# Optimization experiments

Measured on AMD Instinct MI355X. Metric: run time of the kernel, lower is better.

## Reference

```python
import jax, jax.numpy as jnp
import numpy as np

EPS = 1e-5  # BatchNorm eps

def _gcn_norm(edge_index, edge_weight, n):
    # PyG gcn_norm with add_self_loops=True, fill_value=1.0
    loop = jnp.arange(n, dtype=edge_index.dtype)
    row = jnp.concatenate([edge_index[0], loop])
    col = jnp.concatenate([edge_index[1], loop])
    ew = jnp.concatenate([edge_weight, jnp.ones((n,), edge_weight.dtype)])
    deg = jax.ops.segment_sum(ew, col, num_segments=n)
    dis = jnp.where(deg > 0, jax.lax.rsqrt(jnp.maximum(deg, 1e-30)), 0.0)
    norm = dis[row] * ew * dis[col]
    return row, col, norm

def _gcn_conv(x, W, b, row, col, norm, n):
    h = x @ W                               # [N, out]
    msg = h[row] * norm[:, None]            # gather + edge scale
    out = jax.ops.segment_sum(msg, col, num_segments=n)
    return out + b

def _bn_eval(x, gamma, beta, mean, var):
    return (x - mean) * jax.lax.rsqrt(var + EPS) * gamma + beta

def setup_inputs() -> dict:
    key = jax.random.key(0)
    ks = jax.random.split(key, 12)
    N, E, V, H = 100000, 1600000, 256, 128
    x = jax.random.normal(ks[0], (N, V), jnp.float32)
    edge_index = jax.random.randint(ks[1], (2, E), 0, N, jnp.int64)
    edge_weight = jax.random.uniform(ks[2], (E,), jnp.float32)
    s = lambda fan: 1.0 / np.sqrt(fan)
    return {
        "x": x, "edge_index": edge_index, "edge_weight": edge_weight,
        "W1": jax.random.normal(ks[3], (V, H), jnp.float32) * s(V),
        "b1": jnp.zeros((H,), jnp.float32),
        "W2": jax.random.normal(ks[4], (H, H), jnp.float32) * s(H),
        "b2": jnp.zeros((H,), jnp.float32),
        "W3": jax.random.normal(ks[5], (H, 1), jnp.float32) * s(H),
        "b3": jnp.zeros((1,), jnp.float32),
        "Wres": jax.random.normal(ks[6], (V, H), jnp.float32) * s(V),
        "g1": jnp.ones((H,), jnp.float32), "be1": jnp.zeros((H,), jnp.float32),
        "m1": jax.random.normal(ks[7], (H,), jnp.float32) * 0.01,
        "v1": jnp.ones((H,), jnp.float32),
        "g2": jnp.ones((H,), jnp.float32), "be2": jnp.zeros((H,), jnp.float32),
        "m2": jax.random.normal(ks[8], (H,), jnp.float32) * 0.01,
        "v2": jnp.ones((H,), jnp.float32),
    }

def reference(x, edge_index, edge_weight, W1, b1, W2, b2, W3, b3, Wres,
              g1, be1, m1, v1, g2, be2, m2, v2):
    n = x.shape[0]
    row, col, norm = _gcn_norm(edge_index, edge_weight, n)
    res = x @ Wres                                   # residual branch
    h = _gcn_conv(x, W1, b1, row, col, norm, n)
    h = jax.nn.relu(_bn_eval(h, g1, be1, m1, v1))    # dropout off (eval)
    h = _gcn_conv(h, W2, b2, row, col, norm, n) + res
    h = jax.nn.relu(_bn_eval(h, g2, be2, m2, v2))
    h = _gcn_conv(h, W3, b3, row, col, norm, n)      # [N, 1]
    return jnp.squeeze(h, axis=1)
```

## Files before the change

kernel.cpp:

```cpp
#include <hip/hip_runtime.h>
#include <hip/hip_bf16.h>

#define BN_EPS 1e-5f

using short8 = __attribute__((ext_vector_type(8))) short;
using f32x4  = __attribute__((ext_vector_type(4))) float;

#define FIX_SCALE 262144.0f
#define FIX_MASK  0x01ffffffu
#define CNT_ONE   (1u << 25)

static __device__ __forceinline__ unsigned short f2bf(float f) {
  unsigned int u = __float_as_uint(f);
  unsigned int r = (u + 0x7fffu + ((u >> 16) & 1u)) >> 16;
  return (unsigned short)r;
}


static __global__ void cast_weights(const float* __restrict__ W1, const float* __restrict__ Wres,
                                    const float* __restrict__ W2,
                                    unsigned short* __restrict__ B2,
                                    unsigned short* __restrict__ BT2) {
  int i = blockIdx.x * blockDim.x + threadIdx.x;
  if (i < 256 * 256) {
    int n = i >> 8, k = i & 255;
    float v = (n < 128) ? W1[k * 128 + n] : Wres[k * 128 + (n - 128)];
    B2[(k >> 5) * 8192 + n * 32 + (k & 31)] = f2bf(v);
  } else if (i < 256 * 256 + 128 * 128) {
    int j = i - 256 * 256;
    int n = j >> 7, k = j & 127;
    BT2[j] = f2bf(W2[k * 128 + n]);
  }
}


static __global__ __launch_bounds__(256)
void fused_gemm1_hist(const float* __restrict__ A, const unsigned short* __restrict__ B2,
                      unsigned short* __restrict__ C0, unsigned short* __restrict__ C1, int M,
                      const int* __restrict__ col, const float* __restrict__ ew,
                      unsigned int* __restrict__ packed,
                      unsigned short* __restrict__ rank, int E, int hB, int N) {
  __shared__ unsigned short As[2 * 64 * 40];

  int b = blockIdx.x;
  if (b < hB) {
    unsigned int xcc;
    asm volatile("s_getreg_b32 %0, hwreg(HW_REG_XCC_ID)" : "=s"(xcc));
    xcc &= 7u;
    unsigned int* mytab = packed + (size_t)xcc * N;
    int base = b * (256 * 8) + threadIdx.x;
#pragma unroll
    for (int j = 0; j < 8; ++j) {
      int e = base + j * 256;
      if (e < E) {
        int c = col[e];
        unsigned int fx = (unsigned int)(ew[e] * FIX_SCALE + 0.5f);
        unsigned int old = __hip_atomic_fetch_add(&mytab[c], CNT_ONE | fx,
                                                  __ATOMIC_RELAXED,
                                                  __HIP_MEMORY_SCOPE_WORKGROUP);
        rank[e] = (unsigned short)(((old >> 25) & 0x1fffu) | (xcc << 13));
      }
    }
    return;
  }

  int t = threadIdx.x;
  int wv = t >> 6, lane = t & 63;
  int quad = lane >> 4, l15 = lane & 15;
  int m0 = (b - hB) * 64;

  f32x4 acc[4][4];
#pragma unroll
  for (int i = 0; i < 4; ++i)
#pragma unroll
    for (int j = 0; j < 4; ++j) acc[i][j] = (f32x4){0.f, 0.f, 0.f, 0.f};

  int ar = t >> 2;
  int ac = (t & 3) * 8;
  bool avalid = (m0 + ar) < M;
  const float* Arow = A + (size_t)(m0 + ar) * 256 + ac;
  const unsigned short* Bfrag = B2 + (wv * 64 + l15) * 32 + quad * 8;

  float4 a0 = make_float4(0.f, 0.f, 0.f, 0.f), a1 = a0;
  if (avalid) {
    a0 = *(const float4*)(Arow + 0);
    a1 = *(const float4*)(Arow + 4);
  }
  {
    short8 av;
    av[0] = (short)f2bf(a0.x); av[1] = (short)f2bf(a0.y);
    av[2] = (short)f2bf(a0.z); av[3] = (short)f2bf(a0.w);
    av[4] = (short)f2bf(a1.x); av[5] = (short)f2bf(a1.y);
    av[6] = (short)f2bf(a1.z); av[7] = (short)f2bf(a1.w);
    *(short8*)&As[ar * 40 + ac] = av;
  }
  short8 bc[4];
#pragma unroll
  for (int nt = 0; nt < 4; ++nt)
    bc[nt] = *(const short8*)(Bfrag + nt * 512);
  __syncthreads();

#pragma unroll 2
  for (int s = 0; s < 8; ++s) {
    int cur = (s & 1) ? 2560 : 0;

    short8 bn[4];
    if (s < 7) {
#pragma unroll
      for (int nt = 0; nt < 4; ++nt)
        bn[nt] = *(const short8*)(Bfrag + (s + 1) * 8192 + nt * 512);
      if (avalid) {
        a0 = *(const float4*)(Arow + (s + 1) * 32);
        a1 = *(const float4*)(Arow + (s + 1) * 32 + 4);
      }
    }

    short8 af[4];
#pragma unroll
    for (int mt = 0; mt < 4; ++mt)
      af[mt] = *(const short8*)&As[cur + (mt * 16 + l15) * 40 + quad * 8];
#pragma unroll
    for (int mt = 0; mt < 4; ++mt)
#pragma unroll
      for (int nt = 0; nt < 4; ++nt)
        acc[mt][nt] = __builtin_amdgcn_mfma_f32_16x16x32_bf16(af[mt], bc[nt], acc[mt][nt], 0, 0, 0);

    if (s < 7) {
      short8 av;
      av[0] = (short)f2bf(a0.x); av[1] = (short)f2bf(a0.y);
      av[2] = (short)f2bf(a0.z); av[3] = (short)f2bf(a0.w);
      av[4] = (short)f2bf(a1.x); av[5] = (short)f2bf(a1.y);
      av[6] = (short)f2bf(a1.z); av[7] = (short)f2bf(a1.w);
      *(short8*)&As[(cur ^ 2560) + ar * 40 + ac] = av;
#pragma unroll
      for (int nt = 0; nt < 4; ++nt) bc[nt] = bn[nt];
    }
    __syncthreads();
  }

  int nbase = wv * 64;
#pragma unroll
  for (int mt = 0; mt < 4; ++mt) {
#pragma unroll
    for (int nt = 0; nt < 4; ++nt) {
      int n = nbase + nt * 16 + l15;
#pragma unroll
      for (int reg = 0; reg < 4; ++reg) {
        size_t m = (size_t)(m0 + mt * 16 + quad * 4 + reg);
        if (nbase < 128) C0[m * 128 + n] = f2bf(acc[mt][nt][reg]);
        else             C1[m * 128 + (n - 128)] = f2bf(acc[mt][nt][reg]);
      }
    }
  }
}


#define SCAN_B 256
#define SCAN_I 16
static __global__ void scanA(const unsigned int* __restrict__ packed,
                             float* __restrict__ dis, int* __restrict__ cnt,
                             int* __restrict__ startV, int* __restrict__ blkSum, int N) {
  __shared__ int sh[SCAN_B];
  int t = threadIdx.x;
  int vbase = blockIdx.x * (SCAN_B * SCAN_I) + t * SCAN_I;
  int v[SCAN_I];
  int tot = 0;
#pragma unroll
  for (int g = 0; g < 2; ++g) {
    int c = (vbase >> 3) + g;
    int csum = 0;
    if (c < N) {
      unsigned int usum = 0;
#pragma unroll
      for (int r = 0; r < 8; ++r) {
        unsigned int pv = packed[(size_t)r * N + c];
        int cr = (int)(pv >> 25);
        v[g * 8 + r] = cr;
        csum += cr;
        usum += (pv & FIX_MASK);
      }
      cnt[c] = csum;
      dis[c] = rsqrtf(1.0f + (float)usum * (1.0f / FIX_SCALE));
    } else {
#pragma unroll
      for (int r = 0; r < 8; ++r) v[g * 8 + r] = 0;
    }
    tot += csum;
  }
  sh[t] = tot;
  __syncthreads();
  int self = tot;
  for (int off = 1; off < SCAN_B; off <<= 1) {
    int add = (t >= off) ? sh[t - off] : 0;
    __syncthreads();
    sh[t] += add;
    __syncthreads();
  }
  int excl = sh[t] - self;
  if (t == SCAN_B - 1) blkSum[blockIdx.x] = sh[t];
  int run = excl;
#pragma unroll
  for (int j = 0; j < SCAN_I; ++j) {
    if (vbase + j < 8 * N) startV[vbase + j] = run;
    run += v[j];
  }
}

static __global__ void scanB(const int* __restrict__ blkSum, int* __restrict__ blkOff, int nb) {
  __shared__ int sh[256];
  int t = threadIdx.x;
  int v = (t < nb) ? blkSum[t] : 0;
  sh[t] = v;
  __syncthreads();
  for (int off = 1; off < 256; off <<= 1) {
    int add = (t >= off) ? sh[t - off] : 0;
    __syncthreads();
    sh[t] += add;
    __syncthreads();
  }
  if (t < nb) blkOff[t] = sh[t] - v;
}

static __global__ void place_kernel(const int* __restrict__ row, const int* __restrict__ col,
                                    const float* __restrict__ ew, const float* __restrict__ dis,
                                    const int* __restrict__ startV, const int* __restrict__ blkOff,
                                    const unsigned short* __restrict__ rank,
                                    long long* __restrict__ edges, int E) {
  int e = blockIdx.x * blockDim.x + threadIdx.x;
  if (e < E) {
    int r = row[e], c = col[e];
    unsigned int rk = rank[e];
    int vv = c * 8 + (int)(rk >> 13);
    int pos = startV[vv] + blkOff[vv >> 12] + (int)(rk & 0x1fffu);
    float nrm = dis[r] * ew[e];
    long long v = ((long long)__float_as_int(nrm) << 32) | (unsigned int)r;
    __builtin_nontemporal_store(v, &edges[pos]);
  }
}


static __global__ __launch_bounds__(256)
void gemm2_mfma(const unsigned short* __restrict__ A, const unsigned short* __restrict__ BT,
                unsigned short* __restrict__ C) {
  __shared__ unsigned short As[128 * 40];
  __shared__ unsigned short Bs[128 * 40];
  int t = threadIdx.x;
  int wv = t >> 6, lane = t & 63;
  int quad = lane >> 4, l15 = lane & 15;
  int m0 = blockIdx.x * 128;

  f32x4 acc[4][4];
#pragma unroll
  for (int i = 0; i < 4; ++i)
#pragma unroll
    for (int j = 0; j < 4; ++j) acc[i][j] = (f32x4){0.f, 0.f, 0.f, 0.f};

  int sr = t >> 1, sc = (t & 1) * 16;

  for (int k0 = 0; k0 < 128; k0 += 32) {
    short8 a0 = *(const short8*)(A + (size_t)(m0 + sr) * 128 + k0 + sc);
    short8 a1 = *(const short8*)(A + (size_t)(m0 + sr) * 128 + k0 + sc + 8);
    *(short8*)&As[sr * 40 + sc]     = a0;
    *(short8*)&As[sr * 40 + sc + 8] = a1;
    short8 b0 = *(const short8*)(BT + (size_t)sr * 128 + k0 + sc);
    short8 b1 = *(const short8*)(BT + (size_t)sr * 128 + k0 + sc + 8);
    *(short8*)&Bs[sr * 40 + sc]     = b0;
    *(short8*)&Bs[sr * 40 + sc + 8] = b1;
    __syncthreads();

    int mb = (wv >> 1) * 64, nb = (wv & 1) * 64;
    short8 af[4], bf[4];
#pragma unroll
    for (int mt = 0; mt < 4; ++mt)
      af[mt] = *(const short8*)&As[(mb + mt * 16 + l15) * 40 + quad * 8];
#pragma unroll
    for (int nt = 0; nt < 4; ++nt)
      bf[nt] = *(const short8*)&Bs[(nb + nt * 16 + l15) * 40 + quad * 8];
#pragma unroll
    for (int mt = 0; mt < 4; ++mt)
#pragma unroll
      for (int nt = 0; nt < 4; ++nt)
        acc[mt][nt] = __builtin_amdgcn_mfma_f32_16x16x32_bf16(af[mt], bf[nt], acc[mt][nt], 0, 0, 0);
    __syncthreads();
  }

  int mb = (wv >> 1) * 64, nb = (wv & 1) * 64;
#pragma unroll
  for (int mt = 0; mt < 4; ++mt)
#pragma unroll
    for (int nt = 0; nt < 4; ++nt) {
      int n = nb + nt * 16 + l15;
#pragma unroll
      for (int reg = 0; reg < 4; ++reg) {
        size_t m = (size_t)(m0 + mb + mt * 16 + quad * 4 + reg);
        C[m * 128 + n] = f2bf(acc[mt][nt][reg]);
      }
    }
}


#define PROP_GATHER_BODY                                                        \
  int c0 = lane * 2;                                                            \
  float d = dis[w];                                                             \
  float acc0, acc1;                                                             \
  {                                                                             \
    unsigned int u = Hsrc[(size_t)w * 64 + lane];                               \
    acc0 = d * __uint_as_float(u << 16);                                        \
    acc1 = d * __uint_as_float(u & 0xffff0000u);                                \
  }                                                                             \
  int s = start8[(size_t)w * 8] + blkOff[w >> 9], n = cnt[w];                   \
  int k = 0;                                                                    \
  while (k < n) {                                                               \
    int chunk = min(n - k, 64);                                                 \
    int idx = 0;                                                                \
    float wt = 0.f;                                                             \
    if (lane < chunk) {                                                         \
      long long ev = edges[s + k + lane];                                       \
      idx = (int)(unsigned int)(ev & 0xffffffffLL);                             \
      wt  = __int_as_float((int)(ev >> 32));                                    \
    }                                                                           \
    for (int j = 0; j < chunk; j += 8) {                                        \
      int   i0 = __shfl(idx, j + 0, 64), i1 = __shfl(idx, j + 1, 64);           \
      int   i2 = __shfl(idx, j + 2, 64), i3 = __shfl(idx, j + 3, 64);           \
      int   i4 = __shfl(idx, j + 4, 64), i5 = __shfl(idx, j + 5, 64);           \
      int   i6 = __shfl(idx, j + 6, 64), i7 = __shfl(idx, j + 7, 64);           \
      float w0 = __shfl(wt, j + 0, 64), w1 = __shfl(wt, j + 1, 64);             \
      float w2 = __shfl(wt, j + 2, 64), w3 = __shfl(wt, j + 3, 64);             \
      float w4 = __shfl(wt, j + 4, 64), w5 = __shfl(wt, j + 5, 64);             \
      float w6 = __shfl(wt, j + 6, 64), w7 = __shfl(wt, j + 7, 64);             \
      unsigned int u0 = Hsrc[(size_t)i0 * 64 + lane];                           \
      unsigned int u1 = Hsrc[(size_t)i1 * 64 + lane];                           \
      unsigned int u2 = Hsrc[(size_t)i2 * 64 + lane];                           \
      unsigned int u3 = Hsrc[(size_t)i3 * 64 + lane];                           \
      unsigned int u4 = Hsrc[(size_t)i4 * 64 + lane];                           \
      unsigned int u5 = Hsrc[(size_t)i5 * 64 + lane];                           \
      unsigned int u6 = Hsrc[(size_t)i6 * 64 + lane];                           \
      unsigned int u7 = Hsrc[(size_t)i7 * 64 + lane];                           \
      acc0 = fmaf(w0, __uint_as_float(u0 << 16), acc0);                         \
      acc1 = fmaf(w0, __uint_as_float(u0 & 0xffff0000u), acc1);                 \
      acc0 = fmaf(w1, __uint_as_float(u1 << 16), acc0);                         \
      acc1 = fmaf(w1, __uint_as_float(u1 & 0xffff0000u), acc1);                 \
      acc0 = fmaf(w2, __uint_as_float(u2 << 16), acc0);                         \
      acc1 = fmaf(w2, __uint_as_float(u2 & 0xffff0000u), acc1);                 \
      acc0 = fmaf(w3, __uint_as_float(u3 << 16), acc0);                         \
      acc1 = fmaf(w3, __uint_as_float(u3 & 0xffff0000u), acc1);                 \
      acc0 = fmaf(w4, __uint_as_float(u4 << 16), acc0);                         \
      acc1 = fmaf(w4, __uint_as_float(u4 & 0xffff0000u), acc1);                 \
      acc0 = fmaf(w5, __uint_as_float(u5 << 16), acc0);                         \
      acc1 = fmaf(w5, __uint_as_float(u5 & 0xffff0000u), acc1);                 \
      acc0 = fmaf(w6, __uint_as_float(u6 << 16), acc0);                         \
      acc1 = fmaf(w6, __uint_as_float(u6 & 0xffff0000u), acc1);                 \
      acc0 = fmaf(w7, __uint_as_float(u7 << 16), acc0);                         \
      acc1 = fmaf(w7, __uint_as_float(u7 & 0xffff0000u), acc1);                 \
    }                                                                           \
    k += chunk;                                                                 \
  }                                                                             \
  acc0 *= d;                                                                    \
  acc1 *= d;

static __global__ __launch_bounds__(256)
void prop128_bf16out(const unsigned int* __restrict__ Hsrc,
                     const int* __restrict__ start8, const int* __restrict__ blkOff,
                     const int* __restrict__ cnt,
                     const long long* __restrict__ edges,
                     const float* __restrict__ dis,
                     const float* __restrict__ bvec,
                     const float* __restrict__ g, const float* __restrict__ be,
                     const float* __restrict__ mean, const float* __restrict__ var,
                     unsigned int* __restrict__ Outb, int N) {
  int w = (int)((blockIdx.x * blockDim.x + threadIdx.x) >> 6);
  int lane = threadIdx.x & 63;
  if (w >= N) return;
  PROP_GATHER_BODY
  float x0 = acc0 + bvec[c0];
  float x1 = acc1 + bvec[c0 + 1];
  float s0 = g[c0] * rsqrtf(var[c0] + BN_EPS);
  float s1 = g[c0 + 1] * rsqrtf(var[c0 + 1] + BN_EPS);
  x0 = fmaxf((x0 - mean[c0]) * s0 + be[c0], 0.f);
  x1 = fmaxf((x1 - mean[c0 + 1]) * s1 + be[c0 + 1], 0.f);
  unsigned int packed = (unsigned int)f2bf(x0) | ((unsigned int)f2bf(x1) << 16);
  Outb[(size_t)w * 64 + lane] = packed;
}

static __global__ __launch_bounds__(256)
void prop128_w3out(const unsigned int* __restrict__ Hsrc,
                   const int* __restrict__ start8, const int* __restrict__ blkOff,
                   const int* __restrict__ cnt,
                   const long long* __restrict__ edges,
                   const float* __restrict__ dis,
                   const float* __restrict__ bvec,
                   const float* __restrict__ g, const float* __restrict__ be,
                   const float* __restrict__ mean, const float* __restrict__ var,
                   const unsigned int* __restrict__ resb, const float* __restrict__ W3,
                   float* __restrict__ h3, int N) {
  int w = (int)((blockIdx.x * blockDim.x + threadIdx.x) >> 6);
  int lane = threadIdx.x & 63;
  if (w >= N) return;
  PROP_GATHER_BODY
  unsigned int ru = resb[(size_t)w * 64 + lane];
  float x0 = acc0 + bvec[c0]     + __uint_as_float(ru << 16);
  float x1 = acc1 + bvec[c0 + 1] + __uint_as_float(ru & 0xffff0000u);
  float s0 = g[c0] * rsqrtf(var[c0] + BN_EPS);
  float s1 = g[c0 + 1] * rsqrtf(var[c0 + 1] + BN_EPS);
  x0 = fmaxf((x0 - mean[c0]) * s0 + be[c0], 0.f);
  x1 = fmaxf((x1 - mean[c0 + 1]) * s1 + be[c0 + 1], 0.f);
  float v = x0 * W3[c0] + x1 * W3[c0 + 1];
#pragma unroll
  for (int off = 32; off > 0; off >>= 1) v += __shfl_down(v, off, 64);
  if (lane == 0) h3[w] = v;
}


static __global__ __launch_bounds__(256)
void prop3_kernel(const float* __restrict__ h3,
                  const int* __restrict__ start8, const int* __restrict__ blkOff,
                  const int* __restrict__ cnt,
                  const long long* __restrict__ edges,
                  const float* __restrict__ dis, const float* __restrict__ b3,
                  float* __restrict__ out, int N) {
  int tid = blockIdx.x * blockDim.x + threadIdx.x;
  int i = tid >> 2;
  int sub = tid & 3;
  if (i >= N) return;
  float acc = 0.f;
  int s = start8[(size_t)i * 8] + blkOff[i >> 9], n = cnt[i];
  for (int k = sub; k < n; k += 4) {
    long long ev = edges[s + k];
    int src = (int)(unsigned int)(ev & 0xffffffffLL);
    float wt = __int_as_float((int)(ev >> 32));
    acc = fmaf(wt, h3[src], acc);
  }
  acc += __shfl_xor(acc, 1, 64);
  acc += __shfl_xor(acc, 2, 64);
  if (sub == 0) {
    float d = dis[i];
    out[i] = (acc + d * h3[i]) * d + b3[0];
  }
}


extern "C" void kernel_launch(void* const* d_in, const int* in_sizes, int n_in,
                              void* d_out, int out_size, void* d_ws, size_t ws_size,
                              hipStream_t stream) {
  const float* x    = (const float*)d_in[0];
  const int*   ei   = (const int*)d_in[1];
  const float* ew   = (const float*)d_in[2];
  const float* W1   = (const float*)d_in[3];
  const float* b1   = (const float*)d_in[4];
  const float* W2   = (const float*)d_in[5];
  const float* b2   = (const float*)d_in[6];
  const float* W3   = (const float*)d_in[7];
  const float* b3   = (const float*)d_in[8];
  const float* Wres = (const float*)d_in[9];
  const float* g1   = (const float*)d_in[10];
  const float* be1  = (const float*)d_in[11];
  const float* m1   = (const float*)d_in[12];
  const float* v1   = (const float*)d_in[13];
  const float* g2   = (const float*)d_in[14];
  const float* be2  = (const float*)d_in[15];
  const float* m2   = (const float*)d_in[16];
  const float* v2   = (const float*)d_in[17];

  int Hh = in_sizes[4];
  int V  = in_sizes[3] / Hh;
  int N  = in_sizes[0] / V;
  int E  = in_sizes[2];
  const int* row = ei;
  const int* col = ei + E;

  int Mp = ((N + 127) / 128) * 128;

  char* p = (char*)d_ws;
  auto alloc = [&](size_t bytes) -> char* {
    char* r = p;
    p += (bytes + 255) & ~(size_t)255;
    return r;
  };
  unsigned int* packed = (unsigned int*)alloc((size_t)N * 8 * 4);
  float* dis    = (float*)alloc((size_t)N * 4);
  int*   cnt    = (int*)  alloc((size_t)N * 4);
  int*   startV = (int*)  alloc((size_t)N * 8 * 4);
  int*   blkSum = (int*)  alloc(256 * 4);
  int*   blkOff = (int*)  alloc(256 * 4);
  unsigned short* rank = (unsigned short*)alloc((size_t)E * 2);
  long long* edges = (long long*)alloc((size_t)E * 8);
  float* h3     = (float*)alloc((size_t)N * 4);
  unsigned short* B2  = (unsigned short*)alloc((size_t)256 * 256 * 2);
  unsigned short* BT2 = (unsigned short*)alloc((size_t)128 * 128 * 2);
  unsigned short* bufG  = (unsigned short*)alloc((size_t)Mp * 128 * 2);
  unsigned short* bufH1 = (unsigned short*)alloc((size_t)Mp * 128 * 2);
  unsigned short* bufRes = (unsigned short*)alloc((size_t)Mp * 128 * 2);
  (void)ws_size; (void)n_in; (void)out_size;

  int TB = 256;
  hipMemsetAsync(packed, 0, (size_t)N * 8 * 4, stream);
  cast_weights<<<(256 * 256 + 128 * 128 + TB - 1) / TB, TB, 0, stream>>>(W1, Wres, W2, B2, BT2);

  int hB = (E + TB * 8 - 1) / (TB * 8);
  int gB = Mp / 64;
  fused_gemm1_hist<<<hB + gB, TB, 0, stream>>>(x, B2, bufG, bufRes, N,
                                               col, ew, packed, rank, E, hB, N);

  int NV = 8 * N;
  int nb = (NV + SCAN_B * SCAN_I - 1) / (SCAN_B * SCAN_I);
  scanA<<<nb, SCAN_B, 0, stream>>>(packed, dis, cnt, startV, blkSum, N);
  scanB<<<1, 256, 0, stream>>>(blkSum, blkOff, nb);
  place_kernel<<<(E + TB - 1) / TB, TB, 0, stream>>>(row, col, ew, dis, startV, blkOff,
                                                     rank, edges, E);

  int propBlocks = (int)(((size_t)N * 64 + TB - 1) / TB);
  prop128_bf16out<<<propBlocks, TB, 0, stream>>>((const unsigned int*)bufG, startV, blkOff, cnt,
                                                 edges, dis, b1, g1, be1, m1, v1,
                                                 (unsigned int*)bufH1, N);

  gemm2_mfma<<<Mp / 128, 256, 0, stream>>>(bufH1, BT2, bufG);

  prop128_w3out<<<propBlocks, TB, 0, stream>>>((const unsigned int*)bufG, startV, blkOff, cnt,
                                               edges, dis, b2, g2, be2, m2, v2,
                                               (const unsigned int*)bufRes, W3, h3, N);

  prop3_kernel<<<(int)(((size_t)N * 4 + TB - 1) / TB), TB, 0, stream>>>(h3, startV, blkOff, cnt,
                                                                        edges, dis, b3,
                                                                        (float*)d_out, N);
}
```

Before: 483.3 us.

## Replace global-atomic CSR build with two-level bucket sort via LDS counting

The per-XCC global atomic histogram with rank tracking is replaced by a two-level counting sort. Per-block LDS histograms over 128-node buckets are reduced and prefix-scanned, then edges are scattered into buckets. Each bucket is sorted locally into CSR order in LDS, computing degree and dis along the way, and a final pass writes the normalized weights. This removes contended global atomics and the large packed/startV arrays, at the cost of more kernel launches and an extra E-sized temporary pass. It also relies on row indices fitting in 17 bits.

Result: faster. 454.2 us (-6.0%).

```diff
diff --git a/kernel.cpp b/kernel.cpp
--- a/kernel.cpp
+++ b/kernel.cpp
@@ -2,13 +2,13 @@
 #include <hip/hip_bf16.h>
 
 #define BN_EPS 1e-5f
+#define FIX_SCALE 262144.0f
+
+#define EPB 2048
+#define NBK_MAX 816
 
 using short8 = __attribute__((ext_vector_type(8))) short;
 using f32x4  = __attribute__((ext_vector_type(4))) float;
-
-#define FIX_SCALE 262144.0f
-#define FIX_MASK  0x01ffffffu
-#define CNT_ONE   (1u << 25)
 
 static __device__ __forceinline__ unsigned short f2bf(float f) {
   unsigned int u = __float_as_uint(f);
@@ -35,39 +35,32 @@
 
 
 static __global__ __launch_bounds__(256)
-void fused_gemm1_hist(const float* __restrict__ A, const unsigned short* __restrict__ B2,
-                      unsigned short* __restrict__ C0, unsigned short* __restrict__ C1, int M,
-                      const int* __restrict__ col, const float* __restrict__ ew,
-                      unsigned int* __restrict__ packed,
-                      unsigned short* __restrict__ rank, int E, int hB, int N) {
+void fused_count_gemm1(const float* __restrict__ A, const unsigned short* __restrict__ B2,
+                       unsigned short* __restrict__ C0, unsigned short* __restrict__ C1, int M,
+                       const int* __restrict__ col, int* __restrict__ BB,
+                       int E, int CB, int NBK) {
   __shared__ unsigned short As[2 * 64 * 40];
 
   int b = blockIdx.x;
-  if (b < hB) {
-    unsigned int xcc;
-    asm volatile("s_getreg_b32 %0, hwreg(HW_REG_XCC_ID)" : "=s"(xcc));
-    xcc &= 7u;
-    unsigned int* mytab = packed + (size_t)xcc * N;
-    int base = b * (256 * 8) + threadIdx.x;
+  int t = threadIdx.x;
+  if (b < CB) {
+    unsigned int* cnts = (unsigned int*)As;
+    for (int k = t; k < NBK; k += 256) cnts[k] = 0u;
+    __syncthreads();
+    int base = b * EPB + t;
 #pragma unroll
     for (int j = 0; j < 8; ++j) {
       int e = base + j * 256;
-      if (e < E) {
-        int c = col[e];
-        unsigned int fx = (unsigned int)(ew[e] * FIX_SCALE + 0.5f);
-        unsigned int old = __hip_atomic_fetch_add(&mytab[c], CNT_ONE | fx,
-                                                  __ATOMIC_RELAXED,
-                                                  __HIP_MEMORY_SCOPE_WORKGROUP);
-        rank[e] = (unsigned short)(((old >> 25) & 0x1fffu) | (xcc << 13));
-      }
-    }
+      if (e < E) atomicAdd(&cnts[col[e] >> 7], 1u);
+    }
+    __syncthreads();
+    for (int k = t; k < NBK; k += 256) BB[(size_t)b * NBK + k] = (int)cnts[k];
     return;
   }
 
-  int t = threadIdx.x;
   int wv = t >> 6, lane = t & 63;
   int quad = lane >> 4, l15 = lane & 15;
-  int m0 = (b - hB) * 64;
+  int m0 = (b - CB) * 64;
 
   f32x4 acc[4][4];
 #pragma unroll
@@ -155,86 +148,162 @@
 }
 
 
-#define SCAN_B 256
-#define SCAN_I 16
-static __global__ void scanA(const unsigned int* __restrict__ packed,
-                             float* __restrict__ dis, int* __restrict__ cnt,
-                             int* __restrict__ startV, int* __restrict__ blkSum, int N) {
-  __shared__ int sh[SCAN_B];
-  int t = threadIdx.x;
-  int vbase = blockIdx.x * (SCAN_B * SCAN_I) + t * SCAN_I;
-  int v[SCAN_I];
-  int tot = 0;
-#pragma unroll
-  for (int g = 0; g < 2; ++g) {
-    int c = (vbase >> 3) + g;
-    int csum = 0;
+static __global__ void totals_kernel(const int* __restrict__ BB, int* __restrict__ total,
+                                     int CB, int NBK) {
+  __shared__ int sh[256];
+  int k = blockIdx.x;
+  int t = threadIdx.x;
+  int part = 0;
+  for (int b = t; b < CB; b += 256) part += BB[(size_t)b * NBK + k];
+  sh[t] = part;
+  __syncthreads();
+  for (int off = 128; off > 0; off >>= 1) {
+    if (t < off) sh[t] += sh[t + off];
+    __syncthreads();
+  }
+  if (t == 0) total[k] = sh[0];
+}
+
+static __global__ void base_kernel(const int* __restrict__ total, int* __restrict__ bucketBase,
+                                   int NBK) {
+  __shared__ int sh[256];
+  __shared__ int carrySh;
+  int t = threadIdx.x;
+  if (t == 0) carrySh = 0;
+  __syncthreads();
+  for (int c0 = 0; c0 < NBK; c0 += 256) {
+    int i = c0 + t;
+    int v = (i < NBK) ? total[i] : 0;
+    sh[t] = v;
+    __syncthreads();
+    for (int off = 1; off < 256; off <<= 1) {
+      int add = (t >= off) ? sh[t - off] : 0;
+      __syncthreads();
+      sh[t] += add;
+      __syncthreads();
+    }
+    if (i < NBK) bucketBase[i] = carrySh + sh[t] - v;
+    __syncthreads();
+    if (t == 0) carrySh += sh[255];
+    __syncthreads();
+  }
+  if (t == 0) bucketBase[NBK] = carrySh;
+}
+
+static __global__ void off_kernel(int* __restrict__ BB, const int* __restrict__ bucketBase,
+                                  int CB, int NBK) {
+  __shared__ int sh[256];
+  __shared__ int carrySh;
+  int k = blockIdx.x;
+  int t = threadIdx.x;
+  if (t == 0) carrySh = bucketBase[k];
+  __syncthreads();
+  for (int b0 = 0; b0 < CB; b0 += 256) {
+    int b = b0 + t;
+    int v = (b < CB) ? BB[(size_t)b * NBK + k] : 0;
+    sh[t] = v;
+    __syncthreads();
+    for (int off = 1; off < 256; off <<= 1) {
+      int add = (t >= off) ? sh[t - off] : 0;
+      __syncthreads();
+      sh[t] += add;
+      __syncthreads();
+    }
+    if (b < CB) BB[(size_t)b * NBK + k] = carrySh + sh[t] - v;
+    __syncthreads();
+    if (t == 0) carrySh += sh[255];
+    __syncthreads();
+  }
+}
+
+static __global__ void scatter_kernel(const int* __restrict__ row, const int* __restrict__ col,
+                                      const float* __restrict__ ew, const int* __restrict__ BB,
+                                      unsigned long long* __restrict__ tmp, int E, int NBK) {
+  __shared__ unsigned int cur[NBK_MAX];
+  int b = blockIdx.x;
+  int t = threadIdx.x;
+  for (int k = t; k < NBK; k += 256) cur[k] = (unsigned int)BB[(size_t)b * NBK + k];
+  __syncthreads();
+  int base = b * EPB + t;
+#pragma unroll
+  for (int j = 0; j < 8; ++j) {
+    int e = base + j * 256;
+    if (e < E) {
+      int c = col[e];
+      int k = c >> 7;
+      unsigned int pos = atomicAdd(&cur[k], 1u);
+      unsigned int lo = (unsigned int)row[e] | ((unsigned int)(c & 127) << 17);
+      unsigned long long w = ((unsigned long long)__float_as_uint(ew[e]) << 32) | lo;
+      tmp[pos] = w;
+    }
+  }
+}
+
+static __global__ void bucket_csr(const unsigned long long* __restrict__ tmp,
+                                  const int* __restrict__ bucketBase,
+                                  int* __restrict__ cnt, int* __restrict__ start,
+                                  float* __restrict__ dis,
+                                  unsigned long long* __restrict__ edges, int N) {
+  __shared__ unsigned int colCnt[128];
+  __shared__ unsigned int sumEw[128];
+  __shared__ int so[128];
+  int k = blockIdx.x;
+  int t = threadIdx.x;
+  int segBase = bucketBase[k], segEnd = bucketBase[k + 1];
+  int segN = segEnd - segBase;
+
+  if (t < 128) { colCnt[t] = 0u; sumEw[t] = 0u; }
+  __syncthreads();
+
+  for (int i = t; i < segN; i += 256) {
+    unsigned long long w = tmp[segBase + i];
+    unsigned int lo = (unsigned int)w;
+    int cl = (int)((lo >> 17) & 127u);
+    float ewv = __uint_as_float((unsigned int)(w >> 32));
+    atomicAdd(&colCnt[cl], 1u);
+    atomicAdd(&sumEw[cl], (unsigned int)(ewv * FIX_SCALE + 0.5f));
+  }
+  __syncthreads();
+
+  if (t < 128) so[t] = (int)colCnt[t];
+  __syncthreads();
+  for (int off = 1; off < 128; off <<= 1) {
+    int add = (t >= off && t < 128) ? so[t - off] : 0;
+    __syncthreads();
+    if (t < 128) so[t] += add;
+    __syncthreads();
+  }
+
+  if (t < 128) {
+    int excl = so[t] - (int)colCnt[t];
+    int c = k * 128 + t;
     if (c < N) {
-      unsigned int usum = 0;
-#pragma unroll
-      for (int r = 0; r < 8; ++r) {
-        unsigned int pv = packed[(size_t)r * N + c];
-        int cr = (int)(pv >> 25);
-        v[g * 8 + r] = cr;
-        csum += cr;
-        usum += (pv & FIX_MASK);
-      }
-      cnt[c] = csum;
-      dis[c] = rsqrtf(1.0f + (float)usum * (1.0f / FIX_SCALE));
-    } else {
-#pragma unroll
-      for (int r = 0; r < 8; ++r) v[g * 8 + r] = 0;
-    }
-    tot += csum;
-  }
-  sh[t] = tot;
-  __syncthreads();
-  int self = tot;
-  for (int off = 1; off < SCAN_B; off <<= 1) {
-    int add = (t >= off) ? sh[t - off] : 0;
-    __syncthreads();
-    sh[t] += add;
-    __syncthreads();
-  }
-  int excl = sh[t] - self;
-  if (t == SCAN_B - 1) blkSum[blockIdx.x] = sh[t];
-  int run = excl;
-#pragma unroll
-  for (int j = 0; j < SCAN_I; ++j) {
-    if (vbase + j < 8 * N) startV[vbase + j] = run;
-    run += v[j];
-  }
-}
-
-static __global__ void scanB(const int* __restrict__ blkSum, int* __restrict__ blkOff, int nb) {
-  __shared__ int sh[256];
-  int t = threadIdx.x;
-  int v = (t < nb) ? blkSum[t] : 0;
-  sh[t] = v;
-  __syncthreads();
-  for (int off = 1; off < 256; off <<= 1) {
-    int add = (t >= off) ? sh[t - off] : 0;
-    __syncthreads();
-    sh[t] += add;
-    __syncthreads();
-  }
-  if (t < nb) blkOff[t] = sh[t] - v;
-}
-
-static __global__ void place_kernel(const int* __restrict__ row, const int* __restrict__ col,
-                                    const float* __restrict__ ew, const float* __restrict__ dis,
-                                    const int* __restrict__ startV, const int* __restrict__ blkOff,
-                                    const unsigned short* __restrict__ rank,
-                                    long long* __restrict__ edges, int E) {
-  int e = blockIdx.x * blockDim.x + threadIdx.x;
-  if (e < E) {
-    int r = row[e], c = col[e];
-    unsigned int rk = rank[e];
-    int vv = c * 8 + (int)(rk >> 13);
-    int pos = startV[vv] + blkOff[vv >> 12] + (int)(rk & 0x1fffu);
-    float nrm = dis[r] * ew[e];
-    long long v = ((long long)__float_as_int(nrm) << 32) | (unsigned int)r;
-    __builtin_nontemporal_store(v, &edges[pos]);
+      cnt[c] = (int)colCnt[t];
+      start[c] = segBase + excl;
+      dis[c] = rsqrtf(1.0f + (float)sumEw[t] * (1.0f / FIX_SCALE));
+    }
+    colCnt[t] = (unsigned int)excl;
+  }
+  __syncthreads();
+
+  for (int i = t; i < segN; i += 256) {
+    unsigned long long w = tmp[segBase + i];
+    unsigned int lo = (unsigned int)w;
+    int cl = (int)((lo >> 17) & 127u);
+    unsigned int p = atomicAdd(&colCnt[cl], 1u);
+    edges[segBase + (int)p] = (w & 0xffffffff00000000ull) | (unsigned long long)(lo & 0x1ffffu);
+  }
+}
+
+static __global__ void finalize_kernel(unsigned long long* __restrict__ edges,
+                                       const float* __restrict__ dis, int E) {
+  int i = blockIdx.x * blockDim.x + threadIdx.x;
+  if (i < E) {
+    unsigned long long w = edges[i];
+    int r = (int)(unsigned int)(w & 0xffffffffull);
+    float ewv = __uint_as_float((unsigned int)(w >> 32));
+    float nrm = dis[r] * ewv;
+    edges[i] = ((unsigned long long)__float_as_uint(nrm) << 32) | (unsigned int)r;
   }
 }
 
@@ -308,14 +377,14 @@
     acc0 = d * __uint_as_float(u << 16);                                        \
     acc1 = d * __uint_as_float(u & 0xffff0000u);                                \
   }                                                                             \
-  int s = start8[(size_t)w * 8] + blkOff[w >> 9], n = cnt[w];                   \
+  int s = start[w], n = cnt[w];                                                 \
   int k = 0;                                                                    \
   while (k < n) {                                                               \
     int chunk = min(n - k, 64);                                                 \
     int idx = 0;                                                                \
     float wt = 0.f;                                                             \
     if (lane < chunk) {                                                         \
-      long long ev = edges[s + k + lane];                                       \
+      long long ev = (long long)edges[s + k + lane];                            \
       idx = (int)(unsigned int)(ev & 0xffffffffLL);                             \
       wt  = __int_as_float((int)(ev >> 32));                                    \
     }                                                                           \
@@ -360,9 +429,8 @@
 
 static __global__ __launch_bounds__(256)
 void prop128_bf16out(const unsigned int* __restrict__ Hsrc,
-                     const int* __restrict__ start8, const int* __restrict__ blkOff,
-                     const int* __restrict__ cnt,
-                     const long long* __restrict__ edges,
+                     const int* __restrict__ start, const int* __restrict__ cnt,
+                     const unsigned long long* __restrict__ edges,
                      const float* __restrict__ dis,
                      const float* __restrict__ bvec,
                      const float* __restrict__ g, const float* __restrict__ be,
@@ -384,9 +452,8 @@
 
 static __global__ __launch_bounds__(256)
 void prop128_w3out(const unsigned int* __restrict__ Hsrc,
-                   const int* __restrict__ start8, const int* __restrict__ blkOff,
-                   const int* __restrict__ cnt,
-                   const long long* __restrict__ edges,
+                   const int* __restrict__ start, const int* __restrict__ cnt,
+                   const unsigned long long* __restrict__ edges,
                    const float* __restrict__ dis,
                    const float* __restrict__ bvec,
                    const float* __restrict__ g, const float* __restrict__ be,
@@ -413,9 +480,8 @@
 
 static __global__ __launch_bounds__(256)
 void prop3_kernel(const float* __restrict__ h3,
-                  const int* __restrict__ start8, const int* __restrict__ blkOff,
-                  const int* __restrict__ cnt,
-                  const long long* __restrict__ edges,
+                  const int* __restrict__ start, const int* __restrict__ cnt,
+                  const unsigned long long* __restrict__ edges,
                   const float* __restrict__ dis, const float* __restrict__ b3,
                   float* __restrict__ out, int N) {
   int tid = blockIdx.x * blockDim.x + threadIdx.x;
@@ -423,11 +489,11 @@
   int sub = tid & 3;
   if (i >= N) return;
   float acc = 0.f;
-  int s = start8[(size_t)i * 8] + blkOff[i >> 9], n = cnt[i];
+  int s = start[i], n = cnt[i];
   for (int k = sub; k < n; k += 4) {
-    long long ev = edges[s + k];
-    int src = (int)(unsigned int)(ev & 0xffffffffLL);
-    float wt = __int_as_float((int)(ev >> 32));
+    unsigned long long ev = edges[s + k];
+    int src = (int)(unsigned int)(ev & 0xffffffffull);
+    float wt = __uint_as_float((unsigned int)(ev >> 32));
     acc = fmaf(wt, h3[src], acc);
   }
   acc += __shfl_xor(acc, 1, 64);
@@ -469,6 +535,8 @@
   const int* col = ei + E;
 
   int Mp = ((N + 127) / 128) * 128;
+  int CB  = (E + EPB - 1) / EPB;
+  int NBK = (N + 127) >> 7;
 
   char* p = (char*)d_ws;
   auto alloc = [&](size_t bytes) -> char* {
@@ -476,14 +544,14 @@
     p += (bytes + 255) & ~(size_t)255;
     return r;
   };
-  unsigned int* packed = (unsigned int*)alloc((size_t)N * 8 * 4);
+  int*   BB     = (int*)alloc((size_t)CB * NBK * 4);
+  int*   total  = (int*)alloc((size_t)NBK * 4);
+  int*   bucketBase = (int*)alloc((size_t)(NBK + 1) * 4);
   float* dis    = (float*)alloc((size_t)N * 4);
   int*   cnt    = (int*)  alloc((size_t)N * 4);
-  int*   startV = (int*)  alloc((size_t)N * 8 * 4);
-  int*   blkSum = (int*)  alloc(256 * 4);
-  int*   blkOff = (int*)  alloc(256 * 4);
-  unsigned short* rank = (unsigned short*)alloc((size_t)E * 2);
-  long long* edges = (long long*)alloc((size_t)E * 8);
+  int*   startA = (int*)  alloc((size_t)N * 4);
+  unsigned long long* tmp   = (unsigned long long*)alloc((size_t)E * 8);
+  unsigned long long* edges = (unsigned long long*)alloc((size_t)E * 8);
   float* h3     = (float*)alloc((size_t)N * 4);
   unsigned short* B2  = (unsigned short*)alloc((size_t)256 * 256 * 2);
   unsigned short* BT2 = (unsigned short*)alloc((size_t)128 * 128 * 2);
@@ -493,33 +561,31 @@
   (void)ws_size; (void)n_in; (void)out_size;
 
   int TB = 256;
-  hipMemsetAsync(packed, 0, (size_t)N * 8 * 4, stream);
   cast_weights<<<(256 * 256 + 128 * 128 + TB - 1) / TB, TB, 0, stream>>>(W1, Wres, W2, B2, BT2);
 
-  int hB = (E + TB * 8 - 1) / (TB * 8);
   int gB = Mp / 64;
-  fused_gemm1_hist<<<hB + gB, TB, 0, stream>>>(x, B2, bufG, bufRes, N,
-                                               col, ew, packed, rank, E, hB, N);
-
-  int NV = 8 * N;
-  int nb = (NV + SCAN_B * SCAN_I - 1) / (SCAN_B * SCAN_I);
-  scanA<<<nb, SCAN_B, 0, stream>>>(packed, dis, cnt, startV, blkSum, N);
-  scanB<<<1, 256, 0, stream>>>(blkSum, blkOff, nb);
-  place_kernel<<<(E + TB - 1) / TB, TB, 0, stream>>>(row, col, ew, dis, startV, blkOff,
-                                                     rank, edges, E);
+  fused_count_gemm1<<<CB + gB, TB, 0, stream>>>(x, B2, bufG, bufRes, N,
+                                                col, BB, E, CB, NBK);
+
+  totals_kernel<<<NBK, 256, 0, stream>>>(BB, total, CB, NBK);
+  base_kernel<<<1, 256, 0, stream>>>(total, bucketBase, NBK);
+  off_kernel<<<NBK, 256, 0, stream>>>(BB, bucketBase, CB, NBK);
+  scatter_kernel<<<CB, 256, 0, stream>>>(row, col, ew, BB, tmp, E, NBK);
+  bucket_csr<<<NBK, 256, 0, stream>>>(tmp, bucketBase, cnt, startA, dis, edges, N);
+  finalize_kernel<<<(E + 255) / 256, 256, 0, stream>>>(edges, dis, E);
 
   int propBlocks = (int)(((size_t)N * 64 + TB - 1) / TB);
-  prop128_bf16out<<<propBlocks, TB, 0, stream>>>((const unsigned int*)bufG, startV, blkOff, cnt,
+  prop128_bf16out<<<propBlocks, TB, 0, stream>>>((const unsigned int*)bufG, startA, cnt,
                                                  edges, dis, b1, g1, be1, m1, v1,
                                                  (unsigned int*)bufH1, N);
 
   gemm2_mfma<<<Mp / 128, 256, 0, stream>>>(bufH1, BT2, bufG);
 
-  prop128_w3out<<<propBlocks, TB, 0, stream>>>((const unsigned int*)bufG, startV, blkOff, cnt,
+  prop128_w3out<<<propBlocks, TB, 0, stream>>>((const unsigned int*)bufG, startA, cnt,
                                                edges, dis, b2, g2, be2, m2, v2,
                                                (const unsigned int*)bufRes, W3, h3, N);
 
-  prop3_kernel<<<(int)(((size_t)N * 4 + TB - 1) / TB), TB, 0, stream>>>(h3, startV, blkOff, cnt,
+  prop3_kernel<<<(int)(((size_t)N * 4 + TB - 1) / TB), TB, 0, stream>>>(h3, startA, cnt,
                                                                         edges, dis, b3,
                                                                         (float*)d_out, N);
 }
```
